# Optimization experiments

Measured on AMD Instinct MI355X. Metric: run time of the kernel, lower is better.

The kernel has to match this reference:

```python
import jax, jax.numpy as jnp
import numpy as np

N_WORD, N_TOPIC, N_DOC = 30000, 512, 10000
E_WT, E_WD, E_TD = 262144, 262144, 131072
D_IN, D_OUT = 256, 256


def _mean_agg(msg, dst, n):
    # scatter-mean: sum of messages / in-degree (0 for isolated nodes via max(deg,1))
    s = jax.ops.segment_sum(msg, dst, num_segments=n)
    deg = jax.ops.segment_sum(jnp.ones((msg.shape[0],), msg.dtype), dst, num_segments=n)
    return s / jnp.maximum(deg, 1.0)[:, None]


def setup_inputs() -> dict:
    key = jax.random.key(0)
    ks = jax.random.split(key, 16)
    inp = {
        "feat_word": jax.random.normal(ks[0], (N_WORD, D_IN), jnp.float32),
        "feat_topic": jax.random.normal(ks[1], (N_TOPIC, D_IN), jnp.float32),
        "feat_doc": jax.random.normal(ks[2], (N_DOC, D_IN), jnp.float32),
        "wt_src": jax.random.randint(ks[3], (E_WT,), 0, N_WORD, jnp.int32),
        "wt_dst": jax.random.randint(ks[4], (E_WT,), 0, N_TOPIC, jnp.int32),
        "wd_src": jax.random.randint(ks[5], (E_WD,), 0, N_WORD, jnp.int32),
        "wd_dst": jax.random.randint(ks[6], (E_WD,), 0, N_DOC, jnp.int32),
        "td_src": jax.random.randint(ks[7], (E_TD,), 0, N_TOPIC, jnp.int32),
        "td_dst": jax.random.randint(ks[8], (E_TD,), 0, N_DOC, jnp.int32),
        "w_wt": jax.random.uniform(ks[9], (E_WT,), jnp.float32),
        "w_wd": jax.random.uniform(ks[10], (E_WD,), jnp.float32),
        "w_td": jax.random.uniform(ks[11], (E_TD,), jnp.float32),
        # per-relation Linear params (torch convention: W [out,in], y = x @ W.T + b)
        "Wt": jax.random.normal(ks[12], (D_OUT, D_IN), jnp.float32) * 0.02,
        "bt": jnp.zeros((D_OUT,), jnp.float32),
        "Wd": jax.random.normal(ks[13], (D_OUT, D_IN), jnp.float32) * 0.02,
        "bd": jnp.zeros((D_OUT,), jnp.float32),
        "Wtd": jax.random.normal(ks[14], (D_OUT, D_IN), jnp.float32) * 0.02,
        "btd": jnp.zeros((D_OUT,), jnp.float32),
    }
    return inp


def reference(feat_word, feat_topic, feat_doc,
              wt_src, wt_dst, wd_src, wd_dst, td_src, td_dst,
              w_wt, w_wd, w_td,
              Wt, bt, Wd, bd, Wtd, btd):
    # per-relation Linear on source node features (computed once per src node)
    Wh_wt = feat_word @ Wt.T + bt    # [N_WORD, D_OUT]
    Wh_wd = feat_word @ Wd.T + bd    # [N_WORD, D_OUT]
    Wh_td = feat_topic @ Wtd.T + btd  # [N_TOPIC, D_OUT]

    # u_mul_e then mean per destination
    h_topic = _mean_agg(Wh_wt[wt_src] * w_wt[:, None], wt_dst, N_TOPIC)
    m_wd = _mean_agg(Wh_wd[wd_src] * w_wd[:, None], wd_dst, N_DOC)
    m_td = _mean_agg(Wh_td[td_src] * w_td[:, None], td_dst, N_DOC)

    # cross-type reducer 'sum'; doc nodes get activation (dropout is eval/identity)
    h_doc = jax.nn.relu(m_wd + m_td)

    # word nodes receive no messages: their 'h' stays the input features
    return feat_word, h_topic, h_doc
```

## Files before the change

kernel.cpp:

```cpp
#include <hip/hip_runtime.h>
#include <hip/hip_bf16.h>

#define N_WORD  30000
#define N_TOPIC 512
#define N_DOC   10000
#define E_WT    262144
#define E_WD    262144
#define E_TD    131072
#define DIM     256
#define WT_BINS 16
#define SB_WT   (N_TOPIC * WT_BINS)
#define CAP_WT  96
#define CAP_WD  72
#define CAP_TD  48

typedef __attribute__((ext_vector_type(8))) short bf16x8;
typedef __attribute__((ext_vector_type(4))) float f32x4;
typedef __attribute__((ext_vector_type(2))) int int2v;
typedef __attribute__((ext_vector_type(4))) int int4v;

__device__ __forceinline__ short f2bf(float f) {
    __hip_bfloat16 h = __float2bfloat16(f);
    short s;
    __builtin_memcpy(&s, &h, 2);
    return s;
}
__device__ __forceinline__ void acc8(float* a, int4v d, float w) {
    #pragma unroll
    for (int k = 0; k < 4; ++k) {
        union { unsigned int u; float f; } lo, hi;
        lo.u = ((unsigned int)d[k]) << 16;
        hi.u = ((unsigned int)d[k]) & 0xffff0000u;
        a[2 * k]     += lo.f * w;
        a[2 * k + 1] += hi.f * w;
    }
}

#define SCATTER_BLOCKS 2560
#define FWCAST_BLOCKS 3750
#define FTCAST_BLOCKS 64
#define WCAST_BLOCKS  96
#define SC_BLOCKS (SCATTER_BLOCKS + FWCAST_BLOCKS + FTCAST_BLOCKS + WCAST_BLOCKS)

__global__ __launch_bounds__(256) void scatter_cast(
    const int* __restrict__ wt_src, const int* __restrict__ wt_dst, const float* __restrict__ w_wt,
    const int* __restrict__ wd_src, const int* __restrict__ wd_dst, const float* __restrict__ w_wd,
    const int* __restrict__ td_src, const int* __restrict__ td_dst, const float* __restrict__ w_td,
    int* __restrict__ cur_wt, int* __restrict__ cur_wd, int* __restrict__ cur_td,
    int2v* __restrict__ pk_wt, int2v* __restrict__ pk_wd, int2v* __restrict__ pk_td,
    const float* __restrict__ feat_word, const float* __restrict__ feat_topic,
    const float* __restrict__ Wt, const float* __restrict__ Wd, const float* __restrict__ Wtd,
    __hip_bfloat16* __restrict__ fw, __hip_bfloat16* __restrict__ ft,
    __hip_bfloat16* __restrict__ wbt, __hip_bfloat16* __restrict__ wbd,
    __hip_bfloat16* __restrict__ wbtd)
{
    int b = blockIdx.x;
    if (b < 1024) {
        int e = b * 256 + (int)threadIdx.x;
        int s = wt_src[e];
        int sb = wt_dst[e] * WT_BINS + (s >> 11);
        int pos = atomicAdd(&cur_wt[sb], 1);
        if (pos < CAP_WT) {
            int2v p; p.x = s; p.y = __float_as_int(w_wt[e]);
            pk_wt[(size_t)sb * CAP_WT + pos] = p;
        }
        return;
    }
    if (b < 2048) {
        int e = (b - 1024) * 256 + (int)threadIdx.x;
        int d = wd_dst[e];
        int pos = atomicAdd(&cur_wd[d], 1);
        if (pos < CAP_WD) {
            int2v p; p.x = wd_src[e]; p.y = __float_as_int(w_wd[e]);
            pk_wd[(size_t)d * CAP_WD + pos] = p;
        }
        return;
    }
    if (b < SCATTER_BLOCKS) {
        int e = (b - 2048) * 256 + (int)threadIdx.x;
        int d = td_dst[e];
        int pos = atomicAdd(&cur_td[d], 1);
        if (pos < CAP_TD) {
            int2v p; p.x = td_src[e]; p.y = __float_as_int(w_td[e]);
            pk_td[(size_t)d * CAP_TD + pos] = p;
        }
        return;
    }
    const float* src;
    unsigned short* dst;
    int local;
    int cb = b - SCATTER_BLOCKS;
    if (cb < FWCAST_BLOCKS) { src = feat_word; local = cb * 256 + (int)threadIdx.x; dst = (unsigned short*)fw; }
    else if (cb < FWCAST_BLOCKS + FTCAST_BLOCKS) {
        src = feat_topic; local = (cb - FWCAST_BLOCKS) * 256 + (int)threadIdx.x; dst = (unsigned short*)ft;
    } else {
        int i = (cb - FWCAST_BLOCKS - FTCAST_BLOCKS) * 256 + (int)threadIdx.x;
        if (i < 8192) { src = Wt; local = i; dst = (unsigned short*)wbt; }
        else if (i < 16384) { src = Wd; local = i - 8192; dst = (unsigned short*)wbd; }
        else { src = Wtd; local = i - 16384; dst = (unsigned short*)wbtd; }
    }
    f32x4 a = *reinterpret_cast<const f32x4*>(src + (size_t)local * 8);
    f32x4 c = *reinterpret_cast<const f32x4*>(src + (size_t)local * 8 + 4);
    bf16x8 r;
    r[0] = f2bf(a[0]); r[1] = f2bf(a[1]); r[2] = f2bf(a[2]); r[3] = f2bf(a[3]);
    r[4] = f2bf(c[0]); r[5] = f2bf(c[1]); r[6] = f2bf(c[2]); r[7] = f2bf(c[3]);
    *reinterpret_cast<bf16x8*>(dst + (size_t)local * 8) = r;
}

#define GATHER_BLOCKS (SB_WT / 4 + 2 * N_DOC / 4)
#define COPY_BLOCKS 3750
#define GC_BLOCKS (GATHER_BLOCKS + COPY_BLOCKS)
__global__ __launch_bounds__(256) void gather_all(
    const __hip_bfloat16* __restrict__ fw, const __hip_bfloat16* __restrict__ ft,
    const int2v* __restrict__ pk_wt, const int* __restrict__ cur_wt,
    const int2v* __restrict__ pk_wd, const int* __restrict__ cur_wd,
    const int2v* __restrict__ pk_td, const int* __restrict__ cur_td,
    float* __restrict__ part, float* __restrict__ part_sumw,
    __hip_bfloat16* __restrict__ agg_wd, float* __restrict__ mw_wd,
    __hip_bfloat16* __restrict__ agg_td, float* __restrict__ mw_td,
    const float* __restrict__ feat_word, float* __restrict__ out_word)
{
    int bb = blockIdx.x;
    int wv = threadIdx.x >> 6;
    int lane = threadIdx.x & 63;
    int l = lane & 31, hi = lane >> 5;

    if (bb >= GATHER_BLOCKS) {
        int i = (bb - GATHER_BLOCKS) * 256 + (int)threadIdx.x;
        f32x4 a = *reinterpret_cast<const f32x4*>(feat_word + (size_t)i * 8);
        f32x4 c = *reinterpret_cast<const f32x4*>(feat_word + (size_t)i * 8 + 4);
        *reinterpret_cast<f32x4*>(out_word + (size_t)i * 8) = a;
        *reinterpret_cast<f32x4*>(out_word + (size_t)i * 8 + 4) = c;
        return;
    }

    const int2v* pk;
    const unsigned short* T;
    int cnt, deg = 0;
    bool is_wt = bb < SB_WT / 4;
    int node, chunk = 0;
    __hip_bfloat16* agg = nullptr;
    float* mw = nullptr;

    if (is_wt) {
        int xcd = bb & 7;
        int idx = bb >> 3;
        chunk = (idx & 1) * 8 + xcd;
        node = (idx >> 1) * 4 + wv;
        int base = node * WT_BINS + chunk;
        cnt = cur_wt[base]; if (cnt > CAP_WT) cnt = CAP_WT;
        pk = pk_wt + (size_t)base * CAP_WT;
        T = (const unsigned short*)fw;
    } else {
        int w2 = (bb - SB_WT / 4) * 4 + wv;
        int rel = w2 >= N_DOC;
        node = rel ? w2 - N_DOC : w2;
        T = (const unsigned short*)(rel ? ft : fw);
        const int2v* pkb = rel ? pk_td : pk_wd;
        const int* cur = rel ? cur_td : cur_wd;
        const int cap = rel ? CAP_TD : CAP_WD;
        agg = rel ? agg_td : agg_wd;
        mw = rel ? mw_td : mw_wd;
        deg = cur[node];
        cnt = deg > cap ? cap : deg;
        pk = pkb + (size_t)node * cap;
    }

    float acc[8] = {0.f, 0.f, 0.f, 0.f, 0.f, 0.f, 0.f, 0.f};
    float sw = 0.f;
    int j = 0;
    for (; j + 8 <= cnt; j += 8) {
        int2v p[8];
        #pragma unroll
        for (int k = 0; k < 8; ++k) p[k] = pk[j + k];
        int4v v[4];
        #pragma unroll
        for (int q = 0; q < 4; ++q) {
            int r = hi ? p[2 * q + 1].x : p[2 * q].x;
            v[q] = *reinterpret_cast<const int4v*>(T + (size_t)r * DIM + l * 8);
        }
        #pragma unroll
        for (int q = 0; q < 4; ++q) {
            float w = __int_as_float(hi ? p[2 * q + 1].y : p[2 * q].y);
            acc8(acc, v[q], w);
            sw += w;
        }
    }
    for (; j + 2 <= cnt; j += 2) {
        int2v p0 = pk[j], p1 = pk[j + 1];
        int r = hi ? p1.x : p0.x;
        float w = __int_as_float(hi ? p1.y : p0.y);
        int4v v = *reinterpret_cast<const int4v*>(T + (size_t)r * DIM + l * 8);
        acc8(acc, v, w);
        sw += w;
    }
    if (j < cnt) {
        int2v p0 = pk[j];
        float w = hi ? 0.f : __int_as_float(p0.y);
        int4v v = *reinterpret_cast<const int4v*>(T + (size_t)p0.x * DIM + l * 8);
        acc8(acc, v, w);
        sw += w;
    }
    #pragma unroll
    for (int k = 0; k < 8; ++k) acc[k] += __shfl_xor(acc[k], 32, 64);
    sw += __shfl_xor(sw, 32, 64);

    if (is_wt) {
        if (hi == 0) {
            float* pdst = part + ((size_t)chunk * N_TOPIC + node) * DIM + l * 8;
            f32x4 r0 = {acc[0], acc[1], acc[2], acc[3]};
            f32x4 r1 = {acc[4], acc[5], acc[6], acc[7]};
            *reinterpret_cast<f32x4*>(pdst) = r0;
            *reinterpret_cast<f32x4*>(pdst + 4) = r1;
        }
        if (lane == 0) part_sumw[chunk * N_TOPIC + node] = sw;
    } else {
        float inv = 1.f / (float)(deg > 1 ? deg : 1);
        if (hi == 0) {
            int4v r;
            #pragma unroll
            for (int k = 0; k < 4; ++k) {
                unsigned int lo = (unsigned short)f2bf(acc[2 * k] * inv);
                unsigned int hb = (unsigned short)f2bf(acc[2 * k + 1] * inv);
                r[k] = (int)((hb << 16) | lo);
            }
            *reinterpret_cast<int4v*>((unsigned short*)agg + (size_t)node * DIM + l * 8) = r;
        }
        if (lane == 0) mw[node] = sw * inv;
    }
}

#define GEMM_BLOCKS (32 + (N_DOC / 16) * 16 / 4)

__device__ __forceinline__ f32x4 tile_mm_g(
    const unsigned short* __restrict__ A, const unsigned short* __restrict__ W,
    int rt, int ct, int lr, int kh, f32x4 acc)
{
    const unsigned short* Ab = A + (size_t)(rt * 16 + lr) * DIM + kh * 8;
    const unsigned short* Wb = W + (size_t)(ct * 16 + lr) * DIM + kh * 8;
    #pragma unroll
    for (int kk = 0; kk < 8; ++kk) {
        bf16x8 a = *reinterpret_cast<const bf16x8*>(Ab + kk * 32);
        bf16x8 b = *reinterpret_cast<const bf16x8*>(Wb + kk * 32);
        acc = __builtin_amdgcn_mfma_f32_16x16x32_bf16(a, b, acc, 0, 0, 0);
    }
    return acc;
}

__global__ __launch_bounds__(256) void gemm_all(
    const float* __restrict__ part, const float* __restrict__ part_sumw,
    const int* __restrict__ cur_wt,
    const __hip_bfloat16* __restrict__ wbt, const float* __restrict__ bt,
    const __hip_bfloat16* __restrict__ agg_wd, const __hip_bfloat16* __restrict__ wbd,
    const float* __restrict__ bd, const float* __restrict__ mw_d1,
    const __hip_bfloat16* __restrict__ agg_td, const __hip_bfloat16* __restrict__ wbtd,
    const float* __restrict__ btd, const float* __restrict__ mw_d2,
    float* __restrict__ out_topic, float* __restrict__ out_doc)
{
    int lane = threadIdx.x & 63;
    int wv = threadIdx.x >> 6;
    int lr = lane & 15, kh = lane >> 4;

    if (blockIdx.x < 32) {
        __shared__ unsigned short A[16][DIM];
        __shared__ float mwv[16];
        __shared__ float invv[16];
        int rt = blockIdx.x;
        int t = threadIdx.x;
        if (t < 16) {
            int node = rt * 16 + t;
            int d = 0;
            float swt = 0.f;
            #pragma unroll
            for (int c = 0; c < WT_BINS; ++c) {
                int v = cur_wt[node * WT_BINS + c];
                d += v > CAP_WT ? CAP_WT : v;
                swt += part_sumw[c * N_TOPIC + node];
            }
            float inv = 1.f / (float)(d > 1 ? d : 1);
            invv[t] = inv;
            mwv[t] = swt * inv;
        }
        __syncthreads();
        for (int i = t; i < 16 * DIM; i += 256) {
            int n = i >> 8, d = i & 255;
            int node = rt * 16 + n;
            float s = 0.f;
            #pragma unroll
            for (int c = 0; c < WT_BINS; ++c)
                s += part[((size_t)c * N_TOPIC + node) * DIM + d];
            A[n][d] = (unsigned short)f2bf(s * invv[n]);
        }
        __syncthreads();
        #pragma unroll
        for (int q = 0; q < 4; ++q) {
            int ct = wv * 4 + q;
            f32x4 acc = {0.f, 0.f, 0.f, 0.f};
            const unsigned short* Ab = &A[lr][kh * 8];
            const unsigned short* Wb = (const unsigned short*)wbt + (size_t)(ct * 16 + lr) * DIM + kh * 8;
            #pragma unroll
            for (int kk = 0; kk < 8; ++kk) {
                bf16x8 a = *reinterpret_cast<const bf16x8*>(Ab + kk * 32);
                bf16x8 b = *reinterpret_cast<const bf16x8*>(Wb + kk * 32);
                acc = __builtin_amdgcn_mfma_f32_16x16x32_bf16(a, b, acc, 0, 0, 0);
            }
            float bb = bt[ct * 16 + lr];
            #pragma unroll
            for (int j = 0; j < 4; ++j) {
                int n = kh * 4 + j;
                out_topic[(size_t)(rt * 16 + n) * DIM + ct * 16 + lr] = acc[j] + bb * mwv[n];
            }
        }
        return;
    }

    int w2 = (blockIdx.x - 32) * 4 + wv;
    int rt = w2 >> 4, ct = w2 & 15;
    f32x4 acc = {0.f, 0.f, 0.f, 0.f};
    acc = tile_mm_g((const unsigned short*)agg_wd, (const unsigned short*)wbd, rt, ct, lr, kh, acc);
    acc = tile_mm_g((const unsigned short*)agg_td, (const unsigned short*)wbtd, rt, ct, lr, kh, acc);
    float bb1 = bd[ct * 16 + lr];
    float bb2 = btd[ct * 16 + lr];
    #pragma unroll
    for (int j = 0; j < 4; ++j) {
        int row = rt * 16 + kh * 4 + j;
        float v = acc[j] + bb1 * mw_d1[row] + bb2 * mw_d2[row];
        out_doc[(size_t)row * DIM + ct * 16 + lr] = fmaxf(v, 0.f);
    }
}

extern "C" void kernel_launch(void* const* d_in, const int* in_sizes, int n_in,
                              void* d_out, int out_size, void* d_ws, size_t ws_size,
                              hipStream_t stream)
{
    const float* feat_word  = (const float*)d_in[0];
    const float* feat_topic = (const float*)d_in[1];
    const int* wt_src = (const int*)d_in[3];
    const int* wt_dst = (const int*)d_in[4];
    const int* wd_src = (const int*)d_in[5];
    const int* wd_dst = (const int*)d_in[6];
    const int* td_src = (const int*)d_in[7];
    const int* td_dst = (const int*)d_in[8];
    const float* w_wt = (const float*)d_in[9];
    const float* w_wd = (const float*)d_in[10];
    const float* w_td = (const float*)d_in[11];
    const float* Wt   = (const float*)d_in[12];
    const float* bt   = (const float*)d_in[13];
    const float* Wd   = (const float*)d_in[14];
    const float* bd   = (const float*)d_in[15];
    const float* Wtd  = (const float*)d_in[16];
    const float* btd  = (const float*)d_in[17];

    char* ws = (char*)d_ws;
    __hip_bfloat16* fw     = (__hip_bfloat16*)(ws + 0);
    __hip_bfloat16* ft     = (__hip_bfloat16*)(ws + 15360000);
    __hip_bfloat16* wbt    = (__hip_bfloat16*)(ws + 15622144);
    __hip_bfloat16* wbd    = (__hip_bfloat16*)(ws + 15753216);
    __hip_bfloat16* wbtd   = (__hip_bfloat16*)(ws + 15884288);
    __hip_bfloat16* agg_wd = (__hip_bfloat16*)(ws + 16277504);
    __hip_bfloat16* agg_td = (__hip_bfloat16*)(ws + 21397504);
    float* part      = (float*)(ws + 26517504);
    float* part_sumw = (float*)(ws + 34906112);
    float* mw_wd     = (float*)(ws + 34940928);
    float* mw_td     = (float*)(ws + 34980928);
    int* cur_wt = (int*)(ws + 35020928);
    int* cur_wd = (int*)(ws + 35053696);
    int* cur_td = (int*)(ws + 35093696);
    int2v* pk_wt = (int2v*)(ws + 35133696);
    int2v* pk_wd = (int2v*)(ws + 41425152);
    int2v* pk_td = (int2v*)(ws + 47185152);

    float* out = (float*)d_out;
    float* out_topic = out + (size_t)N_WORD * DIM;
    float* out_doc   = out + (size_t)(N_WORD + N_TOPIC) * DIM;

    hipMemsetAsync(ws + 35020928, 0, 112768, stream);

    scatter_cast<<<SC_BLOCKS, 256, 0, stream>>>(
        wt_src, wt_dst, w_wt, wd_src, wd_dst, w_wd, td_src, td_dst, w_td,
        cur_wt, cur_wd, cur_td, pk_wt, pk_wd, pk_td,
        feat_word, feat_topic, Wt, Wd, Wtd, fw, ft, wbt, wbd, wbtd);

    gather_all<<<GC_BLOCKS, 256, 0, stream>>>(
        fw, ft,
        pk_wt, cur_wt,
        pk_wd, cur_wd,
        pk_td, cur_td,
        part, part_sumw, agg_wd, mw_wd, agg_td, mw_td,
        feat_word, out);

    gemm_all<<<GEMM_BLOCKS, 256, 0, stream>>>(
        part, part_sumw, cur_wt,
        wbt, bt,
        agg_wd, wbd, bd, mw_wd,
        agg_td, wbtd, btd, mw_td,
        out_topic, out_doc);
}
```

Baseline: 132.3 us.

## Pack edge source and bf16 weight into one int, batch scatter per thread

Edge records shrink from 8-byte (src, fp32 weight) pairs to a single 32-bit word holding the 16-bit source index and a bf16 weight, halving bucket write and read traffic in the scatter and gather kernels. Each scatter thread now handles four edges, issuing its loads and atomics back-to-back so more are in flight and fewer blocks are launched. The workspace layout is recomputed for the smaller buckets. Rounding edge weights to bf16 adds precision loss, and the packing relies on source indices fitting in 16 bits (N_WORD=30000).

```diff
diff --git a/kernel.cpp b/kernel.cpp
--- a/kernel.cpp
+++ b/kernel.cpp
@@ -16,7 +16,6 @@
 
 typedef __attribute__((ext_vector_type(8))) short bf16x8;
 typedef __attribute__((ext_vector_type(4))) float f32x4;
-typedef __attribute__((ext_vector_type(2))) int int2v;
 typedef __attribute__((ext_vector_type(4))) int int4v;
 
 __device__ __forceinline__ short f2bf(float f) {
@@ -24,6 +23,15 @@
     short s;
     __builtin_memcpy(&s, &h, 2);
     return s;
+}
+__device__ __forceinline__ int pack_pw(int s, float w) {
+    return (int)(((unsigned int)s << 16) | (unsigned short)f2bf(w));
+}
+__device__ __forceinline__ int pw_src(int p) { return (int)(((unsigned int)p) >> 16); }
+__device__ __forceinline__ float pw_w(int p) {
+    union { unsigned int u; float f; } x;
+    x.u = ((unsigned int)p) << 16;
+    return x.f;
 }
 __device__ __forceinline__ void acc8(float* a, int4v d, float w) {
     #pragma unroll
@@ -36,7 +44,10 @@
     }
 }
 
-#define SCATTER_BLOCKS 2560
+#define WT_SBLK 256
+#define WD_SBLK 256
+#define TD_SBLK 128
+#define SCATTER_BLOCKS (WT_SBLK + WD_SBLK + TD_SBLK)
 #define FWCAST_BLOCKS 3750
 #define FTCAST_BLOCKS 64
 #define WCAST_BLOCKS  96
@@ -47,7 +58,7 @@
     const int* __restrict__ wd_src, const int* __restrict__ wd_dst, const float* __restrict__ w_wd,
     const int* __restrict__ td_src, const int* __restrict__ td_dst, const float* __restrict__ w_td,
     int* __restrict__ cur_wt, int* __restrict__ cur_wd, int* __restrict__ cur_td,
-    int2v* __restrict__ pk_wt, int2v* __restrict__ pk_wd, int2v* __restrict__ pk_td,
+    int* __restrict__ pk_wt, int* __restrict__ pk_wd, int* __restrict__ pk_td,
     const float* __restrict__ feat_word, const float* __restrict__ feat_topic,
     const float* __restrict__ Wt, const float* __restrict__ Wd, const float* __restrict__ Wtd,
     __hip_bfloat16* __restrict__ fw, __hip_bfloat16* __restrict__ ft,
@@ -55,35 +66,58 @@
     __hip_bfloat16* __restrict__ wbtd)
 {
     int b = blockIdx.x;
-    if (b < 1024) {
-        int e = b * 256 + (int)threadIdx.x;
-        int s = wt_src[e];
-        int sb = wt_dst[e] * WT_BINS + (s >> 11);
-        int pos = atomicAdd(&cur_wt[sb], 1);
-        if (pos < CAP_WT) {
-            int2v p; p.x = s; p.y = __float_as_int(w_wt[e]);
-            pk_wt[(size_t)sb * CAP_WT + pos] = p;
-        }
+    if (b < WT_SBLK) {
+        int e0 = b * 1024 + (int)threadIdx.x;
+        int s[4], sb[4], pos[4];
+        float wv[4];
+        #pragma unroll
+        for (int k = 0; k < 4; ++k) {
+            int e = e0 + k * 256;
+            s[k] = wt_src[e];
+            sb[k] = wt_dst[e] * WT_BINS + (s[k] >> 11);
+            wv[k] = w_wt[e];
+        }
+        #pragma unroll
+        for (int k = 0; k < 4; ++k) pos[k] = atomicAdd(&cur_wt[sb[k]], 1);
+        #pragma unroll
+        for (int k = 0; k < 4; ++k)
+            if (pos[k] < CAP_WT) pk_wt[(size_t)sb[k] * CAP_WT + pos[k]] = pack_pw(s[k], wv[k]);
         return;
     }
-    if (b < 2048) {
-        int e = (b - 1024) * 256 + (int)threadIdx.x;
-        int d = wd_dst[e];
-        int pos = atomicAdd(&cur_wd[d], 1);
-        if (pos < CAP_WD) {
-            int2v p; p.x = wd_src[e]; p.y = __float_as_int(w_wd[e]);
-            pk_wd[(size_t)d * CAP_WD + pos] = p;
-        }
+    if (b < WT_SBLK + WD_SBLK) {
+        int e0 = (b - WT_SBLK) * 1024 + (int)threadIdx.x;
+        int s[4], d[4], pos[4];
+        float wv[4];
+        #pragma unroll
+        for (int k = 0; k < 4; ++k) {
+            int e = e0 + k * 256;
+            s[k] = wd_src[e];
+            d[k] = wd_dst[e];
+            wv[k] = w_wd[e];
+        }
+        #pragma unroll
+        for (int k = 0; k < 4; ++k) pos[k] = atomicAdd(&cur_wd[d[k]], 1);
+        #pragma unroll
+        for (int k = 0; k < 4; ++k)
+            if (pos[k] < CAP_WD) pk_wd[(size_t)d[k] * CAP_WD + pos[k]] = pack_pw(s[k], wv[k]);
         return;
     }
     if (b < SCATTER_BLOCKS) {
-        int e = (b - 2048) * 256 + (int)threadIdx.x;
-        int d = td_dst[e];
-        int pos = atomicAdd(&cur_td[d], 1);
-        if (pos < CAP_TD) {
-            int2v p; p.x = td_src[e]; p.y = __float_as_int(w_td[e]);
-            pk_td[(size_t)d * CAP_TD + pos] = p;
-        }
+        int e0 = (b - WT_SBLK - WD_SBLK) * 1024 + (int)threadIdx.x;
+        int s[4], d[4], pos[4];
+        float wv[4];
+        #pragma unroll
+        for (int k = 0; k < 4; ++k) {
+            int e = e0 + k * 256;
+            s[k] = td_src[e];
+            d[k] = td_dst[e];
+            wv[k] = w_td[e];
+        }
+        #pragma unroll
+        for (int k = 0; k < 4; ++k) pos[k] = atomicAdd(&cur_td[d[k]], 1);
+        #pragma unroll
+        for (int k = 0; k < 4; ++k)
+            if (pos[k] < CAP_TD) pk_td[(size_t)d[k] * CAP_TD + pos[k]] = pack_pw(s[k], wv[k]);
         return;
     }
     const float* src;
@@ -112,9 +146,9 @@
 #define GC_BLOCKS (GATHER_BLOCKS + COPY_BLOCKS)
 __global__ __launch_bounds__(256) void gather_all(
     const __hip_bfloat16* __restrict__ fw, const __hip_bfloat16* __restrict__ ft,
-    const int2v* __restrict__ pk_wt, const int* __restrict__ cur_wt,
-    const int2v* __restrict__ pk_wd, const int* __restrict__ cur_wd,
-    const int2v* __restrict__ pk_td, const int* __restrict__ cur_td,
+    const int* __restrict__ pk_wt, const int* __restrict__ cur_wt,
+    const int* __restrict__ pk_wd, const int* __restrict__ cur_wd,
+    const int* __restrict__ pk_td, const int* __restrict__ cur_td,
     float* __restrict__ part, float* __restrict__ part_sumw,
     __hip_bfloat16* __restrict__ agg_wd, float* __restrict__ mw_wd,
     __hip_bfloat16* __restrict__ agg_td, float* __restrict__ mw_td,
@@ -134,7 +168,7 @@
         return;
     }
 
-    const int2v* pk;
+    const int* pk;
     const unsigned short* T;
     int cnt, deg = 0;
     bool is_wt = bb < SB_WT / 4;
@@ -156,7 +190,7 @@
         int rel = w2 >= N_DOC;
         node = rel ? w2 - N_DOC : w2;
         T = (const unsigned short*)(rel ? ft : fw);
-        const int2v* pkb = rel ? pk_td : pk_wd;
+        const int* pkb = rel ? pk_td : pk_wd;
         const int* cur = rel ? cur_td : cur_wd;
         const int cap = rel ? CAP_TD : CAP_WD;
         agg = rel ? agg_td : agg_wd;
@@ -170,34 +204,34 @@
     float sw = 0.f;
     int j = 0;
     for (; j + 8 <= cnt; j += 8) {
-        int2v p[8];
+        int p[8];
         #pragma unroll
         for (int k = 0; k < 8; ++k) p[k] = pk[j + k];
         int4v v[4];
         #pragma unroll
         for (int q = 0; q < 4; ++q) {
-            int r = hi ? p[2 * q + 1].x : p[2 * q].x;
+            int r = pw_src(hi ? p[2 * q + 1] : p[2 * q]);
             v[q] = *reinterpret_cast<const int4v*>(T + (size_t)r * DIM + l * 8);
         }
         #pragma unroll
         for (int q = 0; q < 4; ++q) {
-            float w = __int_as_float(hi ? p[2 * q + 1].y : p[2 * q].y);
+            float w = pw_w(hi ? p[2 * q + 1] : p[2 * q]);
             acc8(acc, v[q], w);
             sw += w;
         }
     }
     for (; j + 2 <= cnt; j += 2) {
-        int2v p0 = pk[j], p1 = pk[j + 1];
-        int r = hi ? p1.x : p0.x;
-        float w = __int_as_float(hi ? p1.y : p0.y);
+        int p0 = pk[j], p1 = pk[j + 1];
+        int r = pw_src(hi ? p1 : p0);
+        float w = pw_w(hi ? p1 : p0);
         int4v v = *reinterpret_cast<const int4v*>(T + (size_t)r * DIM + l * 8);
         acc8(acc, v, w);
         sw += w;
     }
     if (j < cnt) {
-        int2v p0 = pk[j];
-        float w = hi ? 0.f : __int_as_float(p0.y);
-        int4v v = *reinterpret_cast<const int4v*>(T + (size_t)p0.x * DIM + l * 8);
+        int p0 = pk[j];
+        float w = hi ? 0.f : pw_w(p0);
+        int4v v = *reinterpret_cast<const int4v*>(T + (size_t)pw_src(p0) * DIM + l * 8);
         acc8(acc, v, w);
         sw += w;
     }
@@ -357,24 +391,24 @@
     __hip_bfloat16* wbt    = (__hip_bfloat16*)(ws + 15622144);
     __hip_bfloat16* wbd    = (__hip_bfloat16*)(ws + 15753216);
     __hip_bfloat16* wbtd   = (__hip_bfloat16*)(ws + 15884288);
-    __hip_bfloat16* agg_wd = (__hip_bfloat16*)(ws + 16277504);
-    __hip_bfloat16* agg_td = (__hip_bfloat16*)(ws + 21397504);
-    float* part      = (float*)(ws + 26517504);
-    float* part_sumw = (float*)(ws + 34906112);
-    float* mw_wd     = (float*)(ws + 34940928);
-    float* mw_td     = (float*)(ws + 34980928);
-    int* cur_wt = (int*)(ws + 35020928);
-    int* cur_wd = (int*)(ws + 35053696);
-    int* cur_td = (int*)(ws + 35093696);
-    int2v* pk_wt = (int2v*)(ws + 35133696);
-    int2v* pk_wd = (int2v*)(ws + 41425152);
-    int2v* pk_td = (int2v*)(ws + 47185152);
+    __hip_bfloat16* agg_wd = (__hip_bfloat16*)(ws + 16015360);
+    __hip_bfloat16* agg_td = (__hip_bfloat16*)(ws + 21135360);
+    float* part      = (float*)(ws + 26255360);
+    float* part_sumw = (float*)(ws + 34643968);
+    float* mw_wd     = (float*)(ws + 34676736);
+    float* mw_td     = (float*)(ws + 34716736);
+    int* cur_wt = (int*)(ws + 34756736);
+    int* cur_wd = (int*)(ws + 34789504);
+    int* cur_td = (int*)(ws + 34829504);
+    int* pk_wt = (int*)(ws + 34869504);
+    int* pk_wd = (int*)(ws + 38015232);
+    int* pk_td = (int*)(ws + 40895232);
 
     float* out = (float*)d_out;
     float* out_topic = out + (size_t)N_WORD * DIM;
     float* out_doc   = out + (size_t)(N_WORD + N_TOPIC) * DIM;
 
-    hipMemsetAsync(ws + 35020928, 0, 112768, stream);
+    hipMemsetAsync(ws + 34756736, 0, 112768, stream);
 
     scatter_cast<<<SC_BLOCKS, 256, 0, stream>>>(
         wt_src, wt_dst, w_wt, wd_src, wd_dst, w_wd, td_src, td_dst, w_td,
```

Result: slower. 146.7 us (+10.9%).
